# Performance work log

Hardware: AMD Instinct MI355X
Metric: run time of the kernel (lower is better)

Reference implementation:

```python
import jax, jax.numpy as jnp
import numpy as np
from jax import lax

BN_EPS = 1e-5
B, C_IN, HW = 512, 3, 128  # crop batch, channels, crop size
C1, C2 = 32, 64
DIST_THRESHOLD = 0.55


def setup_inputs() -> dict:
    key = jax.random.key(0)
    ks = jax.random.split(key, 13)
    return {
        "crops": jax.random.normal(ks[0], (B, C_IN, HW, HW), jnp.float32),
        "w1": jax.random.normal(ks[1], (C1, C_IN, 3, 3), jnp.float32) * 0.1,
        "b1": jax.random.normal(ks[2], (C1,), jnp.float32) * 0.1,
        "g1": jax.random.uniform(ks[3], (C1,), jnp.float32),
        "be1": jax.random.normal(ks[4], (C1,), jnp.float32) * 0.1,
        "m1": jax.random.normal(ks[5], (C1,), jnp.float32) * 0.1,
        "v1": jax.random.uniform(ks[6], (C1,), jnp.float32),
        "w2": jax.random.normal(ks[7], (C2, C1, 3, 3), jnp.float32) * 0.05,
        "b2": jax.random.normal(ks[8], (C2,), jnp.float32) * 0.1,
        "g2": jax.random.uniform(ks[9], (C2,), jnp.float32),
        "be2": jax.random.normal(ks[10], (C2,), jnp.float32) * 0.1,
        "m2": jax.random.normal(ks[11], (C2,), jnp.float32) * 0.1,
        "v2": jax.random.uniform(ks[12], (C2,), jnp.float32),
    }


def _conv(x, w, b, stride):
    y = lax.conv_general_dilated(
        x, w, window_strides=(stride, stride), padding=((1, 1), (1, 1)),
        dimension_numbers=("NCHW", "OIHW", "NCHW"))
    return y + b[None, :, None, None]


def _bn(x, gamma, beta, mean, var):
    inv = gamma * lax.rsqrt(var + BN_EPS)
    return x * inv[None, :, None, None] + (beta - mean * inv)[None, :, None, None]


def _maxpool2(x):
    return lax.reduce_window(x, -jnp.inf, lax.max, (1, 1, 2, 2), (1, 1, 2, 2), "VALID")


def reference(crops, w1, b1, g1, be1, m1, v1, w2, b2, g2, be2, m2, v2):
    # layer1: Conv(3->32, s1, p1) + BN + ReLU + MaxPool2  -> [B, 32, 64, 64]
    h = _maxpool2(jax.nn.relu(_bn(_conv(crops, w1, b1, 1), g1, be1, m1, v1)))
    # layer2: Conv(32->64, s2, p1) + BN + Sigmoid + MaxPool2 -> [B, 64, 16, 16]
    feat = _maxpool2(jax.nn.sigmoid(_bn(_conv(h, w2, b2, 2), g2, be2, m2, v2)))
    # per-crop distribution score thresholded as in uniqueDistribution/MLE
    scores = feat.mean(axis=(1, 2, 3))            # [B]
    detected = scores >= DIST_THRESHOLD           # [B] bool
    return feat, scores, detected
```

## Files before the change

kernel.cpp:

```cpp
#include <hip/hip_runtime.h>
#include <math.h>

#define BN_EPS 1e-5f
#define HW_ 128

typedef unsigned short u16_t;
typedef unsigned int u32_t;

typedef __bf16 bf16x8 __attribute__((ext_vector_type(8)));
typedef __bf16 bf16v2 __attribute__((ext_vector_type(2)));
typedef float f32x4 __attribute__((ext_vector_type(4)));
typedef float f32x16 __attribute__((ext_vector_type(16)));
typedef u32_t u32x4 __attribute__((ext_vector_type(4)));
typedef u32_t u32x2 __attribute__((ext_vector_type(2)));
typedef u32x4 u32x4_ma __attribute__((may_alias));
typedef u32x2 u32x2_ma __attribute__((may_alias));
typedef f32x4 f32x4_ma __attribute__((may_alias));

static __device__ __forceinline__ u16_t f2bf(float f) {
    union { __bf16 v; u16_t u; } x;
    x.v = (__bf16)f;
    return x.u;
}
static __device__ __forceinline__ u32_t packbf(float a, float b) {
    union { bf16v2 v; u32_t u; } x;
    bf16v2 p;
    p[0] = (__bf16)a;
    p[1] = (__bf16)b;
    x.v = p;
    return x.u;
}
static __device__ __forceinline__ bf16x8 ld_frag16(const u16_t* p) {
    union { u32x4 u; bf16x8 f; } x;
    x.u = *(const u32x4_ma*)p;
    return x.f;
}
static __device__ __forceinline__ bf16x8 ld_frag32(const u32_t* p) {
    union { u32x4 u; bf16x8 f; } x;
    x.u = *(const u32x4_ma*)p;
    return x.f;
}
static __device__ __forceinline__ bf16x8 asbf(u32x4 u) {
    union { u32x4 u; bf16x8 f; } x;
    x.u = u;
    return x.f;
}

#define WSUM_OFF 0
#define W2R_OFF  512
#define WF_OFF   9728
#define PT_OFF   10496
#define BN1_OFF  13056
#define BN2_OFF  13120
#define WS_TOTAL 13248

#define CI_U32   (36 * 74)

__global__ __launch_bounds__(512) void prep_kernel(
    const float* __restrict__ w1, const float* __restrict__ b1,
    const float* __restrict__ g1, const float* __restrict__ be1,
    const float* __restrict__ m1, const float* __restrict__ v1,
    const float* __restrict__ w2, const float* __restrict__ b2,
    const float* __restrict__ g2, const float* __restrict__ be2,
    const float* __restrict__ m2, const float* __restrict__ v2,
    u32_t* __restrict__ ws)
{
    const int gtid = blockIdx.x * 512 + threadIdx.x;

    if (gtid < 512) ws[WSUM_OFF + gtid] = 0u;

    for (int idx = gtid; idx < 9216; idx += 8192) {
        int H   = idx / 4608;
        int rem = idx - H * 4608;
        int tap = rem >> 9;
        int r2  = rem & 511;
        int ocl = r2 >> 4;
        int icp = r2 & 15;
        const float* wp = w2 + (H * 32 + ocl) * 288 + tap;
        ws[W2R_OFF + idx] = packbf(wp[(2 * icp) * 9], wp[(2 * icp + 1) * 9]);
    }
    if (gtid < 192) {
        int s = gtid >> 6, lane = gtid & 63;
        int n32 = lane & 31, h = lane >> 5;
        u32x4 f;
        #pragma unroll
        for (int jp = 0; jp < 4; ++jp) {
            int j0 = 2 * jp, j1 = 2 * jp + 1;
            int kx0 = 2 * h + (j0 >> 2), ch0 = j0 & 3;
            int kx1 = 2 * h + (j1 >> 2), ch1 = j1 & 3;
            float va = (kx0 < 3 && ch0 < 3) ? w1[n32 * 27 + ch0 * 9 + s * 3 + kx0] : 0.f;
            float vb = (kx1 < 3 && ch1 < 3) ? w1[n32 * 27 + ch1 * 9 + s * 3 + kx1] : 0.f;
            f[jp] = packbf(va, vb);
        }
        ((u32x4_ma*)(ws + WF_OFF))[gtid] = f;
    }
    if (gtid < 2560) {
        int tt = gtid >> 6, lane = gtid & 63;
        int n32 = lane & 31, h = lane >> 5;
        int gA = n32 >> 2, sub = n32 & 3;
        int pA = tt * 8 + gA;
        int gy = (pA * 241) >> 12; gy = min(gy, 16);
        int gx = min(pA - gy * 17, 16); gx = max(gx, 0);
        int cy = 2 * gy + (sub >> 1), cx = 2 * gx + (sub & 1);
        ws[PT_OFF + gtid] = (u32_t)((cy * 37 + cx + 2 * h) * 2);
    }
    if (gtid >= 1024 && gtid < 1056) {
        int ch = gtid - 1024;
        float inv = g1[ch] * rsqrtf(v1[ch] + BN_EPS);
        float sh  = b1[ch] * inv + be1[ch] - m1[ch] * inv;
        ws[BN1_OFF + 2 * ch]     = __float_as_uint(inv);
        ws[BN1_OFF + 2 * ch + 1] = __float_as_uint(sh);
    }
    if (gtid >= 2048 && gtid < 2112) {
        int ch = gtid - 2048;
        float inv = g2[ch] * rsqrtf(v2[ch] + BN_EPS);
        float sh  = b2[ch] * inv + be2[ch] - m2[ch] * inv;
        ws[BN2_OFF + 2 * ch]     = __float_as_uint(inv);
        ws[BN2_OFF + 2 * ch + 1] = __float_as_uint(sh);
    }
}

__global__ __launch_bounds__(512, 8) void fused_cnn_kernel(
    const float* __restrict__ crops, const u32_t* __restrict__ tab,
    float* __restrict__ out, float* __restrict__ wsum)
{
    __shared__ __align__(16) u32_t uniS[CI_U32];
    __shared__ __align__(16) u16_t hS[289 * 32];
    __shared__ float redS[8];

    const int tid  = threadIdx.x;
    const int wave = tid >> 6;
    const int lane = tid & 63;
    const int quad = lane >> 4;
    const int r    = lane & 15;
    const int n32  = lane & 31;
    const int halfk = lane >> 5;

    const int blk = blockIdx.x;
    const int img = blk >> 4;
    const int t   = blk & 15;
    const int fy0 = (t >> 2) * 4;
    const int fx0 = (t & 3) * 4;
    const int crop_y0 = 8 * fy0 - 3;
    const int crop_x0 = 8 * fx0 - 3;
    const bool interior = (fy0 != 0) && (fx0 != 0);

    const float* cbase = crops + (size_t)img * (3 * HW_ * HW_);
    const int x0a = crop_x0 - 1;
    if (tid < 360) {
        int row = (tid * 6554) >> 16;
        int vec = tid - row * 10;
        int gr  = crop_y0 + row;
        int col0 = x0a + 4 * vec;
        f32x4 c0 = {0.f,0.f,0.f,0.f}, c1 = {0.f,0.f,0.f,0.f}, c2 = {0.f,0.f,0.f,0.f};
        if ((unsigned)gr < 128u) {
            const float* rp = cbase + gr * HW_;
            if (col0 >= 0 && col0 <= 124) {
                c0 = *(const f32x4_ma*)(rp + col0);
                c1 = *(const f32x4_ma*)(rp + HW_ * HW_ + col0);
                c2 = *(const f32x4_ma*)(rp + 2 * HW_ * HW_ + col0);
            } else {
                #pragma unroll
                for (int j = 0; j < 4; ++j) {
                    int gc = col0 + j;
                    if ((unsigned)gc < 128u) {
                        c0[j] = rp[gc];
                        c1[j] = rp[HW_ * HW_ + gc];
                        c2[j] = rp[2 * HW_ * HW_ + gc];
                    }
                }
            }
        }
        const int ccb = 4 * vec - 1;
        u32_t* up = uniS + (row * 37 + ccb) * 2;
        #pragma unroll
        for (int j = 0; j < 4; ++j) {
            if ((unsigned)(ccb + j) < 37u) {
                u32x2 w;
                w[0] = packbf(c0[j], c1[j]);
                w[1] = packbf(c2[j], 0.f);
                *(u32x2_ma*)(up + 2 * j) = w;
            }
        }
    }

    u32x4 wf[3];
    const u32x4_ma* wft = (const u32x4_ma*)(tab + WF_OFF);
    #pragma unroll
    for (int s = 0; s < 3; ++s) wf[s] = wft[s * 64 + lane];
    u32_t pofs[5];
    #pragma unroll
    for (int i = 0; i < 5; ++i) pofs[i] = tab[PT_OFF + (wave + 8 * i) * 64 + lane];
    const float inv1 = __uint_as_float(tab[BN1_OFF + 2 * n32]);
    const float sh1  = __uint_as_float(tab[BN1_OFF + 2 * n32 + 1]);
    __syncthreads();

    const int hsub = n32 & 7;
    const int hchk = n32 >> 3;
    const int pbase = wave * 8 + halfk;

    int hqi[4];
    #pragma unroll
    for (int q = 0; q < 4; ++q)
        hqi[q] = wave * 256 + halfk * 32 + hsub + q * 64 + ((hchk ^ q) << 3);

    const f32x16 z16 = {0.f,0.f,0.f,0.f,0.f,0.f,0.f,0.f,
                        0.f,0.f,0.f,0.f,0.f,0.f,0.f,0.f};

    auto conv_trip = [&](int ii) -> f32x16 {
        const u32_t* bp = uniS + pofs[ii];
        u32x2 l0a = *(const u32x2_ma*)(bp);
        u32x2 l0b = *(const u32x2_ma*)(bp + 2);
        u32x2 l1a = *(const u32x2_ma*)(bp + 74);
        u32x2 l1b = *(const u32x2_ma*)(bp + 76);
        u32x2 l2a = *(const u32x2_ma*)(bp + 148);
        u32x2 l2b = *(const u32x2_ma*)(bp + 150);
        u32x4 a0; a0[0] = l0a[0]; a0[1] = l0a[1]; a0[2] = l0b[0]; a0[3] = l0b[1];
        u32x4 a1; a1[0] = l1a[0]; a1[1] = l1a[1]; a1[2] = l1b[0]; a1[3] = l1b[1];
        u32x4 a2; a2[0] = l2a[0]; a2[1] = l2a[1]; a2[2] = l2b[0]; a2[3] = l2b[1];
        f32x16 acc = __builtin_amdgcn_mfma_f32_32x32x16_bf16(asbf(a0), asbf(wf[0]), z16, 0, 0, 0);
        acc = __builtin_amdgcn_mfma_f32_32x32x16_bf16(asbf(a1), asbf(wf[1]), acc, 0, 0, 0);
        acc = __builtin_amdgcn_mfma_f32_32x32x16_bf16(asbf(a2), asbf(wf[2]), acc, 0, 0, 0);
        return acc;
    };

    auto pool_val = [&](int ii, int q, const f32x16& acc) -> float {
        float m4 = fmaxf(fmaxf(fmaxf(acc[4 * q], acc[4 * q + 1]), acc[4 * q + 2]),
                         acc[4 * q + 3]);
        float val = fmaxf(fmaf(m4, inv1, sh1), 0.f);
        if (!interior) {
            int pD  = pbase + ii * 64 + 2 * q;
            int gyD = (pD * 241) >> 12;
            int gxD = pD - gyD * 17;
            int y2 = 4 * fy0 - 1 + gyD, x2 = 4 * fx0 - 1 + gxD;
            if (y2 < 0 || y2 > 63 || x2 < 0 || x2 > 63) val = 0.f;
        }
        return val;
    };

    #pragma unroll
    for (int i = 0; i < 4; ++i) {
        f32x16 acc = conv_trip(i);
        #pragma unroll
        for (int q = 0; q < 4; ++q)
            hS[hqi[q] + i * 2048] = f2bf(pool_val(i, q, acc));
    }
    if (wave < 4) {
        f32x16 acc = conv_trip(4);
        #pragma unroll
        for (int q = 0; q < 4; ++q)
            hS[hqi[q] + 4 * 2048] = f2bf(pool_val(4, q, acc));
    } else if (wave == 4) {
        f32x16 acc = conv_trip(4);
        float val = pool_val(4, 0, acc);
        if (halfk == 0) hS[hqi[0] + 4 * 2048] = f2bf(val);
    }
    __syncthreads();

    float* outp = out + (size_t)img * 16384;
    const f32x4 zero4 = {0.f, 0.f, 0.f, 0.f};
    const int mt  = wave & 1;
    const int nt0 = wave >> 1;
    const int cy2 = 2 * nt0 + ((r >> 1) & 1);
    const int cx2 = 2 * (r >> 2) + (r & 1);
    const int fy  = fy0 + nt0;
    const int p0  = 34 * cy2 + 2 * cx2;

    const int oc0 = mt * 16 + r;
    const u32_t* wz0 = tab + W2R_OFF + oc0 * 16 + quad * 4;
    const u32_t* wz1 = wz0 + 4608;
    const float s2_0  = __uint_as_float(tab[BN2_OFF + 2 * oc0]);
    const float sh2_0 = __uint_as_float(tab[BN2_OFF + 2 * oc0 + 1]);
    const float s2_1  = __uint_as_float(tab[BN2_OFF + 64 + 2 * oc0]);
    const float sh2_1 = __uint_as_float(tab[BN2_OFF + 64 + 2 * oc0 + 1]);

    auto ld_ah = [&](int p) -> bf16x8 {
        return ld_frag16(&hS[p * 32 + (((quad ^ (p >> 1)) & 3) << 3)]);
    };

    f32x4 acc0 = zero4, acc1 = zero4;
    bf16x8 w0a = ld_frag32(wz0);
    bf16x8 w1a = ld_frag32(wz1);
    bf16x8 w0b = ld_frag32(wz0 + 512);
    bf16x8 w1b = ld_frag32(wz1 + 512);
    bf16x8 ahn = ld_ah(p0);
    #pragma unroll
    for (int s = 0; s < 9; ++s) {
        bf16x8 ah = ahn;
        if (s < 8) {
            const int ns = s + 1;
            const int nky = ns / 3, nkx = ns - 3 * nky;
            ahn = ld_ah(p0 + nky * 17 + nkx);
        }
        bf16x8 cw0 = w0a, cw1 = w1a;
        w0a = w0b; w1a = w1b;
        if (s < 7) {
            w0b = ld_frag32(wz0 + (s + 2) * 512);
            w1b = ld_frag32(wz1 + (s + 2) * 512);
        }
        acc0 = __builtin_amdgcn_mfma_f32_16x16x32_bf16(ah, cw0, acc0, 0, 0, 0);
        acc1 = __builtin_amdgcn_mfma_f32_16x16x32_bf16(ah, cw1, acc1, 0, 0, 0);
    }

    float m40 = fmaxf(fmaxf(fmaxf(acc0[0], acc0[1]), acc0[2]), acc0[3]);
    float z0  = fmaf(m40, s2_0, sh2_0);
    float sig0 = 1.f / (1.f + __expf(-z0));
    outp[oc0 * 256 + fy * 16 + fx0 + quad] = sig0;
    float m41 = fmaxf(fmaxf(fmaxf(acc1[0], acc1[1]), acc1[2]), acc1[3]);
    float z1  = fmaf(m41, s2_1, sh2_1);
    float sig1 = 1.f / (1.f + __expf(-z1));
    outp[(32 + oc0) * 256 + fy * 16 + fx0 + quad] = sig1;
    float ssum = sig0 + sig1;

    #pragma unroll
    for (int off = 32; off > 0; off >>= 1)
        ssum += __shfl_xor(ssum, off);
    if (lane == 0) redS[wave] = ssum;
    __syncthreads();
    if (tid == 0) {
        float bs = 0.f;
        #pragma unroll
        for (int w = 0; w < 8; ++w) bs += redS[w];
        atomicAdd(&wsum[img], bs);
    }
}

__global__ void finalize_kernel(const float* __restrict__ ws,
                                float* __restrict__ scores,
                                float* __restrict__ detected) {
    int i = threadIdx.x;
    float mean = ws[i] * (1.f / 16384.f);
    scores[i] = mean;
    detected[i] = (mean >= 0.55f) ? 1.f : 0.f;
}

extern "C" void kernel_launch(void* const* d_in, const int* in_sizes, int n_in,
                              void* d_out, int out_size, void* d_ws, size_t ws_size,
                              hipStream_t stream) {
    (void)in_sizes; (void)n_in; (void)out_size; (void)ws_size;
    const float* crops = (const float*)d_in[0];
    const float* w1  = (const float*)d_in[1];
    const float* b1  = (const float*)d_in[2];
    const float* g1  = (const float*)d_in[3];
    const float* be1 = (const float*)d_in[4];
    const float* m1  = (const float*)d_in[5];
    const float* v1  = (const float*)d_in[6];
    const float* w2  = (const float*)d_in[7];
    const float* b2  = (const float*)d_in[8];
    const float* g2  = (const float*)d_in[9];
    const float* be2 = (const float*)d_in[10];
    const float* m2  = (const float*)d_in[11];
    const float* v2  = (const float*)d_in[12];
    float* out = (float*)d_out;
    u32_t* ws  = (u32_t*)d_ws;

    prep_kernel<<<16, 512, 0, stream>>>(
        w1, b1, g1, be1, m1, v1, w2, b2, g2, be2, m2, v2, ws);
    fused_cnn_kernel<<<8192, 512, 0, stream>>>(
        crops, ws, out, (float*)ws);
    finalize_kernel<<<1, 512, 0, stream>>>(
        (const float*)ws, out + 8388608, out + 8388608 + 512);
}
```

Baseline: 266.6 us.

## Loop each block over four x-tiles with register prefetch of next crop tile

```diff
diff --git a/kernel.cpp b/kernel.cpp
--- a/kernel.cpp
+++ b/kernel.cpp
@@ -137,52 +137,44 @@
     const int halfk = lane >> 5;
 
     const int blk = blockIdx.x;
-    const int img = blk >> 4;
-    const int t   = blk & 15;
-    const int fy0 = (t >> 2) * 4;
-    const int fx0 = (t & 3) * 4;
+    const int img = blk >> 2;
+    const int fy0 = (blk & 3) * 4;
     const int crop_y0 = 8 * fy0 - 3;
-    const int crop_x0 = 8 * fx0 - 3;
-    const bool interior = (fy0 != 0) && (fx0 != 0);
 
     const float* cbase = crops + (size_t)img * (3 * HW_ * HW_);
-    const int x0a = crop_x0 - 1;
-    if (tid < 360) {
-        int row = (tid * 6554) >> 16;
-        int vec = tid - row * 10;
-        int gr  = crop_y0 + row;
-        int col0 = x0a + 4 * vec;
-        f32x4 c0 = {0.f,0.f,0.f,0.f}, c1 = {0.f,0.f,0.f,0.f}, c2 = {0.f,0.f,0.f,0.f};
-        if ((unsigned)gr < 128u) {
-            const float* rp = cbase + gr * HW_;
-            if (col0 >= 0 && col0 <= 124) {
-                c0 = *(const f32x4_ma*)(rp + col0);
-                c1 = *(const f32x4_ma*)(rp + HW_ * HW_ + col0);
-                c2 = *(const f32x4_ma*)(rp + 2 * HW_ * HW_ + col0);
-            } else {
-                #pragma unroll
-                for (int j = 0; j < 4; ++j) {
-                    int gc = col0 + j;
-                    if ((unsigned)gc < 128u) {
-                        c0[j] = rp[gc];
-                        c1[j] = rp[HW_ * HW_ + gc];
-                        c2[j] = rp[2 * HW_ * HW_ + gc];
-                    }
+    const bool act = (tid < 360);
+    const int row = (tid * 6554) >> 16;
+    const int vec = tid - row * 10;
+    const int gr  = crop_y0 + row;
+    const bool grv = (unsigned)gr < 128u;
+    const float* rp = cbase + gr * HW_;
+    const int ccb = 4 * vec - 1;
+    u32_t* const up = uniS + (row * 37 + ccb) * 2;
+
+    auto pf = [&](int k, f32x4& a0, f32x4& a1, f32x4& a2) {
+        f32x4 z = {0.f, 0.f, 0.f, 0.f};
+        a0 = z; a1 = z; a2 = z;
+        int col0 = 32 * k - 4 + 4 * vec;
+        if (act && grv && col0 >= 0 && col0 <= 124) {
+            const float* p = rp + col0;
+            a0 = *(const f32x4_ma*)p;
+            a1 = *(const f32x4_ma*)(p + HW_ * HW_);
+            a2 = *(const f32x4_ma*)(p + 2 * HW_ * HW_);
+        }
+    };
+    auto st = [&](const f32x4& a0, const f32x4& a1, const f32x4& a2) {
+        if (act) {
+            #pragma unroll
+            for (int j = 0; j < 4; ++j) {
+                if ((unsigned)(ccb + j) < 37u) {
+                    u32x2 w;
+                    w[0] = packbf(a0[j], a1[j]);
+                    w[1] = packbf(a2[j], 0.f);
+                    *(u32x2_ma*)(up + 2 * j) = w;
                 }
             }
         }
-        const int ccb = 4 * vec - 1;
-        u32_t* up = uniS + (row * 37 + ccb) * 2;
-        #pragma unroll
-        for (int j = 0; j < 4; ++j) {
-            if ((unsigned)(ccb + j) < 37u) {
-                u32x2 w;
-                w[0] = packbf(c0[j], c1[j]);
-                w[1] = packbf(c2[j], 0.f);
-                *(u32x2_ma*)(up + 2 * j) = w;
-            }
-        }
-    }
+    };
 
     u32x4 wf[3];
     const u32x4_ma* wft = (const u32x4_ma*)(tab + WF_OFF);
@@ -193,12 +185,26 @@
     for (int i = 0; i < 5; ++i) pofs[i] = tab[PT_OFF + (wave + 8 * i) * 64 + lane];
     const float inv1 = __uint_as_float(tab[BN1_OFF + 2 * n32]);
     const float sh1  = __uint_as_float(tab[BN1_OFF + 2 * n32 + 1]);
-    __syncthreads();
+
+    float* outp = out + (size_t)img * 16384;
+    const f32x4 zero4 = {0.f, 0.f, 0.f, 0.f};
+    const int mt  = wave & 1;
+    const int nt0 = wave >> 1;
+    const int cy2 = 2 * nt0 + ((r >> 1) & 1);
+    const int cx2 = 2 * (r >> 2) + (r & 1);
+    const int fy  = fy0 + nt0;
+    const int p0  = 34 * cy2 + 2 * cx2;
+    const int oc0 = mt * 16 + r;
+    const u32_t* wz0 = tab + W2R_OFF + oc0 * 16 + quad * 4;
+    const u32_t* wz1 = wz0 + 4608;
+    const float s2_0  = __uint_as_float(tab[BN2_OFF + 2 * oc0]);
+    const float sh2_0 = __uint_as_float(tab[BN2_OFF + 2 * oc0 + 1]);
+    const float s2_1  = __uint_as_float(tab[BN2_OFF + 64 + 2 * oc0]);
+    const float sh2_1 = __uint_as_float(tab[BN2_OFF + 64 + 2 * oc0 + 1]);
 
     const int hsub = n32 & 7;
     const int hchk = n32 >> 3;
     const int pbase = wave * 8 + halfk;
-
     int hqi[4];
     #pragma unroll
     for (int q = 0; q < 4; ++q)
@@ -224,93 +230,78 @@
         return acc;
     };
 
-    auto pool_val = [&](int ii, int q, const f32x16& acc) -> float {
-        float m4 = fmaxf(fmaxf(fmaxf(acc[4 * q], acc[4 * q + 1]), acc[4 * q + 2]),
-                         acc[4 * q + 3]);
-        float val = fmaxf(fmaf(m4, inv1, sh1), 0.f);
-        if (!interior) {
-            int pD  = pbase + ii * 64 + 2 * q;
-            int gyD = (pD * 241) >> 12;
-            int gxD = pD - gyD * 17;
-            int y2 = 4 * fy0 - 1 + gyD, x2 = 4 * fx0 - 1 + gxD;
-            if (y2 < 0 || y2 > 63 || x2 < 0 || x2 > 63) val = 0.f;
-        }
-        return val;
-    };
-
-    #pragma unroll
-    for (int i = 0; i < 4; ++i) {
-        f32x16 acc = conv_trip(i);
+    {
+        f32x4 c0, c1, c2;
+        pf(0, c0, c1, c2);
+        st(c0, c1, c2);
+    }
+    __syncthreads();
+
+    float ssum = 0.f;
+
+    for (int k = 0; k < 4; ++k) {
+        const bool inter = (fy0 != 0) && (k != 0);
+
+        f32x4 c0n, c1n, c2n;
+        if (k < 3) pf(k + 1, c0n, c1n, c2n);
+
+        auto pool_val = [&](int ii, int q, const f32x16& acc) -> float {
+            float m4 = fmaxf(fmaxf(fmaxf(acc[4 * q], acc[4 * q + 1]), acc[4 * q + 2]),
+                             acc[4 * q + 3]);
+            float val = fmaxf(fmaf(m4, inv1, sh1), 0.f);
+            if (!inter) {
+                int pD  = pbase + ii * 64 + 2 * q;
+                int gyD = (pD * 241) >> 12;
+                int gxD = pD - gyD * 17;
+                int y2 = 4 * fy0 - 1 + gyD, x2 = 16 * k - 1 + gxD;
+                if (y2 < 0 || y2 > 63 || x2 < 0 || x2 > 63) val = 0.f;
+            }
+            return val;
+        };
+
         #pragma unroll
-        for (int q = 0; q < 4; ++q)
-            hS[hqi[q] + i * 2048] = f2bf(pool_val(i, q, acc));
-    }
-    if (wave < 4) {
-        f32x16 acc = conv_trip(4);
+        for (int i = 0; i < 4; ++i) {
+            f32x16 acc = conv_trip(i);
+            #pragma unroll
+            for (int q = 0; q < 4; ++q)
+                hS[hqi[q] + i * 2048] = f2bf(pool_val(i, q, acc));
+        }
+        if (wave < 4) {
+            f32x16 acc = conv_trip(4);
+            #pragma unroll
+            for (int q = 0; q < 4; ++q)
+                hS[hqi[q] + 4 * 2048] = f2bf(pool_val(4, q, acc));
+        } else if (wave == 4) {
+            f32x16 acc = conv_trip(4);
+            float val = pool_val(4, 0, acc);
+            if (halfk == 0) hS[hqi[0] + 4 * 2048] = f2bf(val);
+        }
+        __syncthreads();
+
+        f32x4 acc0 = zero4, acc1 = zero4;
         #pragma unroll
-        for (int q = 0; q < 4; ++q)
-            hS[hqi[q] + 4 * 2048] = f2bf(pool_val(4, q, acc));
-    } else if (wave == 4) {
-        f32x16 acc = conv_trip(4);
-        float val = pool_val(4, 0, acc);
-        if (halfk == 0) hS[hqi[0] + 4 * 2048] = f2bf(val);
-    }
-    __syncthreads();
-
-    float* outp = out + (size_t)img * 16384;
-    const f32x4 zero4 = {0.f, 0.f, 0.f, 0.f};
-    const int mt  = wave & 1;
-    const int nt0 = wave >> 1;
-    const int cy2 = 2 * nt0 + ((r >> 1) & 1);
-    const int cx2 = 2 * (r >> 2) + (r & 1);
-    const int fy  = fy0 + nt0;
-    const int p0  = 34 * cy2 + 2 * cx2;
-
-    const int oc0 = mt * 16 + r;
-    const u32_t* wz0 = tab + W2R_OFF + oc0 * 16 + quad * 4;
-    const u32_t* wz1 = wz0 + 4608;
-    const float s2_0  = __uint_as_float(tab[BN2_OFF + 2 * oc0]);
-    const float sh2_0 = __uint_as_float(tab[BN2_OFF + 2 * oc0 + 1]);
-    const float s2_1  = __uint_as_float(tab[BN2_OFF + 64 + 2 * oc0]);
-    const float sh2_1 = __uint_as_float(tab[BN2_OFF + 64 + 2 * oc0 + 1]);
-
-    auto ld_ah = [&](int p) -> bf16x8 {
-        return ld_frag16(&hS[p * 32 + (((quad ^ (p >> 1)) & 3) << 3)]);
-    };
-
-    f32x4 acc0 = zero4, acc1 = zero4;
-    bf16x8 w0a = ld_frag32(wz0);
-    bf16x8 w1a = ld_frag32(wz1);
-    bf16x8 w0b = ld_frag32(wz0 + 512);
-    bf16x8 w1b = ld_frag32(wz1 + 512);
-    bf16x8 ahn = ld_ah(p0);
-    #pragma unroll
-    for (int s = 0; s < 9; ++s) {
-        bf16x8 ah = ahn;
-        if (s < 8) {
-            const int ns = s + 1;
-            const int nky = ns / 3, nkx = ns - 3 * nky;
-            ahn = ld_ah(p0 + nky * 17 + nkx);
-        }
-        bf16x8 cw0 = w0a, cw1 = w1a;
-        w0a = w0b; w1a = w1b;
-        if (s < 7) {
-            w0b = ld_frag32(wz0 + (s + 2) * 512);
-            w1b = ld_frag32(wz1 + (s + 2) * 512);
-        }
-        acc0 = __builtin_amdgcn_mfma_f32_16x16x32_bf16(ah, cw0, acc0, 0, 0, 0);
-        acc1 = __builtin_amdgcn_mfma_f32_16x16x32_bf16(ah, cw1, acc1, 0, 0, 0);
-    }
-
-    float m40 = fmaxf(fmaxf(fmaxf(acc0[0], acc0[1]), acc0[2]), acc0[3]);
-    float z0  = fmaf(m40, s2_0, sh2_0);
-    float sig0 = 1.f / (1.f + __expf(-z0));
-    outp[oc0 * 256 + fy * 16 + fx0 + quad] = sig0;
-    float m41 = fmaxf(fmaxf(fmaxf(acc1[0], acc1[1]), acc1[2]), acc1[3]);
-    float z1  = fmaf(m41, s2_1, sh2_1);
-    float sig1 = 1.f / (1.f + __expf(-z1));
-    outp[(32 + oc0) * 256 + fy * 16 + fx0 + quad] = sig1;
-    float ssum = sig0 + sig1;
+        for (int s = 0; s < 9; ++s) {
+            const int ky = s / 3, kx = s - 3 * (s / 3);
+            int p = (2 * cy2 + ky) * 17 + (2 * cx2 + kx);
+            bf16x8 ah = ld_frag16(&hS[p * 32 + (((quad ^ (p >> 1)) & 3) << 3)]);
+            bf16x8 bw0 = ld_frag32(wz0 + s * 512);
+            bf16x8 bw1 = ld_frag32(wz1 + s * 512);
+            acc0 = __builtin_amdgcn_mfma_f32_16x16x32_bf16(ah, bw0, acc0, 0, 0, 0);
+            acc1 = __builtin_amdgcn_mfma_f32_16x16x32_bf16(ah, bw1, acc1, 0, 0, 0);
+        }
+        float m40 = fmaxf(fmaxf(fmaxf(acc0[0], acc0[1]), acc0[2]), acc0[3]);
+        float z0  = fmaf(m40, s2_0, sh2_0);
+        float sig0 = 1.f / (1.f + __expf(-z0));
+        outp[oc0 * 256 + fy * 16 + 4 * k + quad] = sig0;
+        float m41 = fmaxf(fmaxf(fmaxf(acc1[0], acc1[1]), acc1[2]), acc1[3]);
+        float z1  = fmaf(m41, s2_1, sh2_1);
+        float sig1 = 1.f / (1.f + __expf(-z1));
+        outp[(32 + oc0) * 256 + fy * 16 + 4 * k + quad] = sig1;
+        ssum += sig0 + sig1;
+
+        if (k < 3) st(c0n, c1n, c2n);
+        __syncthreads();
+    }
 
     #pragma unroll
     for (int off = 32; off > 0; off >>= 1)
@@ -356,7 +347,7 @@
 
     prep_kernel<<<16, 512, 0, stream>>>(
         w1, b1, g1, be1, m1, v1, w2, b2, g2, be2, m2, v2, ws);
-    fused_cnn_kernel<<<8192, 512, 0, stream>>>(
+    fused_cnn_kernel<<<2048, 512, 0, stream>>>(
         crops, ws, out, (float*)ws);
     finalize_kernel<<<1, 512, 0, stream>>>(
         (const float*)ws, out + 8388608, out + 8388608 + 512);
```

After: 582.6 us. +118.5%, slower.
